# Performance work log

Hardware: AMD Instinct MI355X
Metric: run time of the kernel (lower is better)

Reference implementation:

```python
import jax, jax.numpy as jnp
import numpy as np

B, T, N, E = 4, 16, 1024, 16384
F_IN, H, FF, NH, L, C = 128, 256, 1024, 8, 2, 10
HD = H // NH
EPS = 1e-5


def setup_inputs() -> dict:
    key = jax.random.key(0)
    ks = jax.random.split(key, 12)
    g = lambda k, s: jax.random.normal(k, s, dtype=jnp.float32) * 0.02
    return {
        "x": jax.random.normal(ks[0], (B, T, N, F_IN), dtype=jnp.float32),
        "edge_index": jax.random.randint(ks[1], (B, T, 2, E), 0, N, dtype=jnp.int32),
        # GraphSAGE layer 1 (PyG SAGEConv: lin_l on mean-aggregated neighbors, lin_r on self)
        "sage1_Wl": g(ks[2], (F_IN, H)), "sage1_bl": jnp.zeros((H,), jnp.float32),
        "sage1_Wr": g(ks[3], (F_IN, H)),
        # GraphSAGE layer 2
        "sage2_Wl": g(ks[4], (H, H)), "sage2_bl": jnp.zeros((H,), jnp.float32),
        "sage2_Wr": g(ks[5], (H, H)),
        # TransformerEncoder, stacked over L layers
        "Wqkv": g(ks[6], (L, H, 3 * H)), "bqkv": jnp.zeros((L, 3 * H), jnp.float32),
        "Wo": g(ks[7], (L, H, H)), "bo": jnp.zeros((L, H), jnp.float32),
        "ln1_s": jnp.ones((L, H), jnp.float32), "ln1_b": jnp.zeros((L, H), jnp.float32),
        "W1": g(ks[8], (L, H, FF)), "b1": jnp.zeros((L, FF), jnp.float32),
        "W2": g(ks[9], (L, FF, H)), "b2": jnp.zeros((L, H), jnp.float32),
        "ln2_s": jnp.ones((L, H), jnp.float32), "ln2_b": jnp.zeros((L, H), jnp.float32),
        # final classifier
        "fc_W": g(ks[10], (H, C)), "fc_b": jnp.zeros((C,), jnp.float32),
    }


def _sage_conv(x, src, dst, Wl, bl, Wr):
    # mean neighbor aggregation: for each target node, mean of source features
    deg = jax.ops.segment_sum(jnp.ones((E,), x.dtype), dst, num_segments=N)
    agg = jax.ops.segment_sum(x[src], dst, num_segments=N)  # [N, F]
    agg = agg / jnp.clip(deg, 1.0)[:, None]
    return agg @ Wl + bl + x @ Wr


def _layernorm(x, s, b):
    m = jnp.mean(x, axis=-1, keepdims=True)
    v = jnp.var(x, axis=-1, keepdims=True)
    return (x - m) * jax.lax.rsqrt(v + EPS) * s + b


def _encoder_layer(h, Wqkv, bqkv, Wo, bo, ln1_s, ln1_b, W1, b1, W2, b2, ln2_s, ln2_b):
    # h: [B, T, H] -- post-norm (PyTorch default norm_first=False), relu FFN
    qkv = h @ Wqkv + bqkv  # [B, T, 3H]
    q, k, v = jnp.split(qkv, 3, axis=-1)
    sp = lambda t: t.reshape(B, T, NH, HD).transpose(0, 2, 1, 3)  # [B, NH, T, HD]
    q, k, v = sp(q), sp(k), sp(v)
    scores = jnp.einsum("bhqd,bhkd->bhqk", q, k) / np.sqrt(HD).astype(np.float32)
    attn = jax.nn.softmax(scores, axis=-1)
    ctx = jnp.einsum("bhqk,bhkd->bhqd", attn, v)
    ctx = ctx.transpose(0, 2, 1, 3).reshape(B, T, H)
    h = _layernorm(h + ctx @ Wo + bo, ln1_s, ln1_b)
    ffn = jax.nn.relu(h @ W1 + b1) @ W2 + b2
    return _layernorm(h + ffn, ln2_s, ln2_b)


def reference(x, edge_index, sage1_Wl, sage1_bl, sage1_Wr, sage2_Wl, sage2_bl,
              sage2_Wr, Wqkv, bqkv, Wo, bo, ln1_s, ln1_b, W1, b1, W2, b2,
              ln2_s, ln2_b, fc_W, fc_b):
    xf = x.reshape(B * T, N, F_IN)
    ef = edge_index.reshape(B * T, 2, E)

    def per_graph(xg, eg):
        src, dst = eg[0], eg[1]
        h = jax.nn.relu(_sage_conv(xg, src, dst, sage1_Wl, sage1_bl, sage1_Wr))
        h = _sage_conv(h, src, dst, sage2_Wl, sage2_bl, sage2_Wr)
        return jnp.mean(h, axis=0)  # mean-pool over nodes -> [H]

    emb = jax.vmap(per_graph)(xf, ef).reshape(B, T, H)

    h = emb
    for l in range(L):
        h = _encoder_layer(h, Wqkv[l], bqkv[l], Wo[l], bo[l], ln1_s[l], ln1_b[l],
                           W1[l], b1[l], W2[l], b2[l], ln2_s[l], ln2_b[l])
    return h[:, -1, :] @ fc_W + fc_b  # [B, C]
```

## Files before the change

kernel.cpp:

```cpp
#include <hip/hip_runtime.h>
#include <hip/hip_bf16.h>

#define Bc 4
#define Tc 16
#define Nc 1024
#define Ec 16384
#define FIN 128
#define Hc 256
#define FFc 1024
#define NHc 8
#define Lc 2
#define HDc 32
#define Gc 64
#define EPSc 1e-5f

typedef __bf16 v8bf __attribute__((ext_vector_type(8)));
typedef float v4f __attribute__((ext_vector_type(4)));

#define TREE256(red, tid, OUTVAR) {                                             \
    if ((tid) < 128) red[tid] += red[(tid) + 128];                              \
    __syncthreads();                                                            \
    if ((tid) < 64) {                                                           \
        float v_ = red[tid] + red[(tid) + 64];                                  \
        v_ += __shfl_down(v_, 32);                                              \
        v_ += __shfl_down(v_, 16);                                              \
        v_ += __shfl_down(v_, 8);                                               \
        v_ += __shfl_down(v_, 4);                                               \
        v_ += __shfl_down(v_, 2);                                               \
        v_ += __shfl_down(v_, 1);                                               \
        if ((tid) == 0) red[0] = v_;                                            \
    }                                                                           \
    __syncthreads();                                                            \
    OUTVAR = red[0];                                                            \
}

__global__ void pack_w_kernel(const float* __restrict__ Wl, const float* __restrict__ Wr,
                              __bf16* __restrict__ pH, __bf16* __restrict__ pL) {
    int bid = blockIdx.x;
    int t = threadIdx.x;
    int lane = t >> 3, j = t & 7;
    int kc = bid >> 4, nt = bid & 15;
    int k = kc * 32 + ((lane >> 4) << 3) + j;
    int n = nt * 16 + (lane & 15);
    float w = (k < 128) ? Wl[(size_t)k * Hc + n] : Wr[(size_t)(k - 128) * Hc + n];
    __bf16 hi = (__bf16)w;
    __bf16 lo = (__bf16)(w - (float)hi);
    pH[bid * 512 + t] = hi;
    pL[bid * 512 + t] = lo;
}

__global__ __launch_bounds__(1024) void csr_kernel(
        const int* __restrict__ ei, float* __restrict__ invdeg, float* __restrict__ cw,
        int* __restrict__ off, unsigned short* __restrict__ elist, float* __restrict__ uv) {
    __shared__ int degs[Nc];
    __shared__ float inv[Nc];
    __shared__ float cl[Nc];
    __shared__ int wsum[16];
    int g = blockIdx.x, t = threadIdx.x;
    const int* src = ei + (size_t)g * 2 * Ec;
    const int* dst = src + Ec;
    int ld[16], ls[16];
#pragma unroll
    for (int i = 0; i < 16; ++i) ld[i] = dst[t + i * 1024] & (Nc - 1);
#pragma unroll
    for (int i = 0; i < 16; ++i) ls[i] = src[t + i * 1024] & (Nc - 1);
    if (t < 512) uv[g * 512 + t] = 0.f;
    degs[t] = 0; cl[t] = 0.f;
    __syncthreads();
#pragma unroll
    for (int i = 0; i < 16; ++i) atomicAdd(&degs[ld[i]], 1);
    __syncthreads();
    float iv = 1.0f / fmaxf((float)degs[t], 1.0f);
    inv[t] = iv;
    invdeg[g * Nc + t] = iv;
    __syncthreads();
#pragma unroll
    for (int i = 0; i < 16; ++i) atomicAdd(&cl[ls[i]], inv[ld[i]]);
    __syncthreads();
    cw[g * Nc + t] = cl[t];
    int own = degs[t];
    int lane = t & 63, wv = t >> 6;
    int val = own;
#pragma unroll
    for (int ofs = 1; ofs < 64; ofs <<= 1) {
        int v = __shfl_up(val, ofs, 64);
        if (lane >= ofs) val += v;
    }
    if (lane == 63) wsum[wv] = val;
    __syncthreads();
    if (wv == 0 && lane < 16) {
        int wval = wsum[lane];
#pragma unroll
        for (int ofs = 1; ofs < 16; ofs <<= 1) {
            int v = __shfl_up(wval, ofs, 64);
            if (lane >= ofs) wval += v;
        }
        wsum[lane] = wval;
    }
    __syncthreads();
    int incl = val + ((wv > 0) ? wsum[wv - 1] : 0);
    int excl = incl - own;
    off[g * 1032 + t] = excl;
    if (t == 1023) off[g * 1032 + Nc] = incl;
    degs[t] = excl;
    __syncthreads();
#pragma unroll
    for (int i = 0; i < 16; ++i) {
        int slot = atomicAdd(&degs[ld[i]], 1);
        elist[(size_t)g * Ec + slot] = (unsigned short)ls[i];
    }
}

__global__ __launch_bounds__(512) void sage_kernel(
        const float* __restrict__ x, const unsigned short* __restrict__ elist,
        const int* __restrict__ off, const float* __restrict__ invdeg,
        const float* __restrict__ cw, const __bf16* __restrict__ pH,
        const __bf16* __restrict__ pL, const float* __restrict__ bias,
        float* __restrict__ uv) {
    __shared__ float aggL[32 * 132];
    __shared__ float xL[32 * 132];
    __shared__ float lu[256], lv[256];
    int tid = threadIdx.x;
    int bid = blockIdx.x;
    int g = bid & 63, cc = bid >> 6, r0 = cc * 32;
    const unsigned short* el = elist + (size_t)g * Ec;
    const float* xg = x + (size_t)g * Nc * FIN;
    if (tid < 256) { lu[tid] = 0.f; lv[tid] = 0.f; }

    {
        int lr = tid >> 4, ch = tid & 15;
        int n = r0 + lr;
        int o0 = off[g * 1032 + n], o1 = off[g * 1032 + n + 1];
        float4 a0 = make_float4(0.f, 0.f, 0.f, 0.f);
        float4 a1 = make_float4(0.f, 0.f, 0.f, 0.f);
        const float* xc = xg + ch * 8;
        int e = o0;
        for (; e + 8 <= o1; e += 8) {
            int s[8];
#pragma unroll
            for (int j = 0; j < 8; ++j) s[j] = el[e + j];
            float4 v0[8], v1[8];
#pragma unroll
            for (int j = 0; j < 8; ++j) {
                const float4* xp = (const float4*)(xc + (size_t)s[j] * FIN);
                v0[j] = xp[0]; v1[j] = xp[1];
            }
#pragma unroll
            for (int j = 0; j < 8; ++j) {
                a0.x += v0[j].x; a0.y += v0[j].y; a0.z += v0[j].z; a0.w += v0[j].w;
                a1.x += v1[j].x; a1.y += v1[j].y; a1.z += v1[j].z; a1.w += v1[j].w;
            }
        }
        for (; e < o1; ++e) {
            const float4* xp = (const float4*)(xc + (size_t)el[e] * FIN);
            float4 v0 = xp[0], v1 = xp[1];
            a0.x += v0.x; a0.y += v0.y; a0.z += v0.z; a0.w += v0.w;
            a1.x += v1.x; a1.y += v1.y; a1.z += v1.z; a1.w += v1.w;
        }
        float iv = invdeg[g * Nc + n];
        float* dp = &aggL[lr * 132 + ch * 8];
        dp[0] = a0.x * iv; dp[1] = a0.y * iv; dp[2] = a0.z * iv; dp[3] = a0.w * iv;
        dp[4] = a1.x * iv; dp[5] = a1.y * iv; dp[6] = a1.z * iv; dp[7] = a1.w * iv;
    }
    for (int i = tid; i < 1024; i += 512) {
        int lr = i >> 5, kq = i & 31;
        *(float4*)&xL[lr * 132 + kq * 4] = *(const float4*)&xg[(size_t)(r0 + lr) * FIN + kq * 4];
    }
    __syncthreads();

    int w = tid >> 6, lane = tid & 63, quad = lane >> 4;
    int mt = w & 1, nh = w >> 1;
    int lrow = mt * 16 + (lane & 15);
    v4f acc[4];
#pragma unroll
    for (int i = 0; i < 4; ++i) acc[i] = (v4f)0.f;
    for (int kc = 0; kc < 8; ++kc) {
        const float* ap = (kc < 4) ? &aggL[lrow * 132 + kc * 32 + quad * 8]
                                   : &xL[lrow * 132 + (kc - 4) * 32 + quad * 8];
        float4 f0 = *(const float4*)ap;
        float4 f1 = *(const float4*)(ap + 4);
        float av[8] = {f0.x, f0.y, f0.z, f0.w, f1.x, f1.y, f1.z, f1.w};
        v8bf aH, aL;
#pragma unroll
        for (int j = 0; j < 8; ++j) {
            __bf16 hb = (__bf16)av[j];
            aH[j] = hb;
            aL[j] = (__bf16)(av[j] - (float)hb);
        }
#pragma unroll
        for (int i = 0; i < 4; ++i) {
            int nt = nh * 4 + i;
            v8bf bH = *(const v8bf*)(pH + ((size_t)(kc * 16 + nt) * 64 + lane) * 8);
            v8bf bL = *(const v8bf*)(pL + ((size_t)(kc * 16 + nt) * 64 + lane) * 8);
            acc[i] = __builtin_amdgcn_mfma_f32_16x16x32_bf16(aH, bH, acc[i], 0, 0, 0);
            acc[i] = __builtin_amdgcn_mfma_f32_16x16x32_bf16(aL, bH, acc[i], 0, 0, 0);
            acc[i] = __builtin_amdgcn_mfma_f32_16x16x32_bf16(aH, bL, acc[i], 0, 0, 0);
        }
    }

    float c4[4];
    int nb = g * Nc + r0 + mt * 16 + quad * 4;
#pragma unroll
    for (int r = 0; r < 4; ++r) c4[r] = cw[nb + r];
#pragma unroll
    for (int i = 0; i < 4; ++i) {
        int col = (nh * 4 + i) * 16 + (lane & 15);
        float bcol = bias[col];
        float su = 0.f, sv = 0.f;
#pragma unroll
        for (int r = 0; r < 4; ++r) {
            float val = fmaxf(acc[i][r] + bcol, 0.f);
            sv += val;
            su += c4[r] * val;
        }
        su += __shfl_xor(su, 16); sv += __shfl_xor(sv, 16);
        su += __shfl_xor(su, 32); sv += __shfl_xor(sv, 32);
        if (quad == 0) { atomicAdd(&lu[col], su); atomicAdd(&lv[col], sv); }
    }
    __syncthreads();
    if (tid < 256) {
        atomicAdd(&uv[g * 512 + tid], lu[tid]);
        atomicAdd(&uv[g * 512 + 256 + tid], lv[tid]);
    }
}

__global__ __launch_bounds__(512) void emb_kernel(
        const float* __restrict__ uv, const float* __restrict__ Wl2,
        const float* __restrict__ bl2, const float* __restrict__ Wr2,
        float* __restrict__ h) {
    __shared__ float s[512];
    __shared__ float r2[512];
    int g = blockIdx.x, tid = threadIdx.x;
    s[tid] = uv[g * 512 + tid] * (1.0f / Nc);
    __syncthreads();
    int col = tid & 255, p = tid >> 8;
    float val = 0.f;
    if (p == 0) { for (int k = 0; k < 256; ++k) val += s[k] * Wl2[(size_t)k * Hc + col]; }
    else        { for (int k = 0; k < 256; ++k) val += s[256 + k] * Wr2[(size_t)k * Hc + col]; }
    r2[tid] = val;
    __syncthreads();
    if (tid < 256) h[g * Hc + tid] = bl2[tid] + r2[tid] + r2[tid + 256];
}

__global__ __launch_bounds__(512) void qkv_kernel(
        const float* __restrict__ h, const float* __restrict__ Wqkv,
        const float* __restrict__ bqkv, float* __restrict__ qkv, int l) {
    __shared__ float hr[256];
    __shared__ float r2[512];
    int bid = blockIdx.x;
    int gi = bid / 3, seg = bid % 3;
    int tid = threadIdx.x;
    if (tid < 256) hr[tid] = h[gi * Hc + tid];
    __syncthreads();
    int col = seg * 256 + (tid & 255);
    int half = tid >> 8;
    const float* W = Wqkv + (size_t)l * Hc * 768;
    float val = 0.f;
    int k0 = half * 128;
    for (int k = 0; k < 128; ++k) val += hr[k0 + k] * W[(size_t)(k0 + k) * 768 + col];
    r2[tid] = val;
    __syncthreads();
    if (tid < 256) qkv[gi * 768 + col] = bqkv[(size_t)l * 768 + col] + r2[tid] + r2[tid + 256];
}

#define KVS 516
__global__ __launch_bounds__(1024) void rest_kernel(
        const float* __restrict__ hin, float* __restrict__ hout,
        const float* __restrict__ qkvg,
        const float* __restrict__ Wo, const float* __restrict__ bo,
        const float* __restrict__ s1, const float* __restrict__ b1ln,
        const float* __restrict__ W1, const float* __restrict__ bf1,
        const float* __restrict__ W2, const float* __restrict__ bf2,
        const float* __restrict__ s2, const float* __restrict__ b2ln,
        const float* __restrict__ fcW, const float* __restrict__ fcb,
        float* __restrict__ out, int l, int last) {
    __shared__ float kv[16 * KVS];
    __shared__ float q[256];
    __shared__ float sc[8][17];
    __shared__ float ctx[256];
    __shared__ float r2[512];
    __shared__ float red[256];
    __shared__ float rF[2048];
    __shared__ float fLs[1024];
    __shared__ float h1L[256];
    int t = blockIdx.x, tid = threadIdx.x;
    int b = t >> 4;
    const float* qb = qkvg + (size_t)(b * 16) * 768;
    for (int i = tid; i < 8192; i += 1024) {
        int j = i >> 9, d = i & 511;
        kv[j * KVS + d] = qb[(size_t)j * 768 + 256 + d];
    }
    if (tid < 256) q[tid] = qkvg[(size_t)t * 768 + tid];
    __syncthreads();
    if (tid < 128) {
        int hd = tid >> 4, jj = tid & 15;
        float s = 0.f;
#pragma unroll
        for (int d = 0; d < 32; ++d) s += q[hd * 32 + d] * kv[jj * KVS + hd * 32 + d];
        sc[hd][jj] = s * 0.17677669529663687f;
    }
    __syncthreads();
    if (tid < 8) {
        float m = sc[tid][0];
        for (int j = 1; j < 16; ++j) m = fmaxf(m, sc[tid][j]);
        float e[16], sum = 0.f;
        for (int j = 0; j < 16; ++j) { e[j] = expf(sc[tid][j] - m); sum += e[j]; }
        float inv = 1.0f / sum;
        for (int j = 0; j < 16; ++j) sc[tid][j] = e[j] * inv;
    }
    __syncthreads();
    if (tid < 256) {
        int hd = tid >> 5, d = tid & 31;
        float o = 0.f;
#pragma unroll
        for (int j = 0; j < 16; ++j) o += sc[hd][j] * kv[j * KVS + 256 + hd * 32 + d];
        ctx[tid] = o;
    }
    __syncthreads();
    if (tid < 512) {
        int col = tid & 255, half = tid >> 8;
        const float* W = Wo + (size_t)l * 65536;
        float pv = 0.f;
        int k0 = half * 128;
        for (int k = 0; k < 128; ++k) pv += ctx[k0 + k] * W[(size_t)(k0 + k) * 256 + col];
        r2[tid] = pv;
    }
    __syncthreads();
    float val = 0.f;
    if (tid < 256) {
        val = hin[(size_t)t * 256 + tid] + bo[(size_t)l * 256 + tid] + r2[tid] + r2[tid + 256];
        red[tid] = val;
    }
    __syncthreads();
    float sm1; TREE256(red, tid, sm1);
    float m1 = sm1 * (1.0f / 256.0f);
    __syncthreads();
    float d1 = val - m1;
    if (tid < 256) red[tid] = d1 * d1;
    __syncthreads();
    float sv1; TREE256(red, tid, sv1);
    float v1 = sv1 * (1.0f / 256.0f);
    if (tid < 256)
        h1L[tid] = d1 * rsqrtf(v1 + EPSc) * s1[(size_t)l * 256 + tid] + b1ln[(size_t)l * 256 + tid];
    __syncthreads();
#pragma unroll
    for (int pass = 0; pass < 2; ++pass) {
        int pid = pass * 1024 + tid;
        int cg = pid >> 9, ch = pid & 511;
        int col = cg * 256 + (ch & 255), half = ch >> 8;
        const float* W = W1 + (size_t)l * 262144;
        float v = 0.f;
        int k0 = half * 128;
        for (int k = 0; k < 128; ++k) v += h1L[k0 + k] * W[(size_t)(k0 + k) * 1024 + col];
        rF[pid] = v;
    }
    __syncthreads();
    {
        int cg = tid >> 8, c8 = tid & 255;
        fLs[tid] = fmaxf(bf1[(size_t)l * 1024 + tid] + rF[cg * 512 + c8] + rF[cg * 512 + 256 + c8], 0.f);
    }
    __syncthreads();
    {
        int col = tid & 255, kq = tid >> 8;
        const float* W = W2 + (size_t)l * 262144;
        float p = 0.f;
        int k0 = kq * 256;
        for (int k = 0; k < 256; ++k) p += fLs[k0 + k] * W[(size_t)(k0 + k) * 256 + col];
        rF[tid] = p;
    }
    __syncthreads();
    float val2 = 0.f;
    if (tid < 256) {
        val2 = h1L[tid] + bf2[(size_t)l * 256 + tid]
             + rF[tid] + rF[tid + 256] + rF[tid + 512] + rF[tid + 768];
        red[tid] = val2;
    }
    __syncthreads();
    float sm2; TREE256(red, tid, sm2);
    float m2 = sm2 * (1.0f / 256.0f);
    __syncthreads();
    float d2 = (tid < 256) ? (val2 - m2) : 0.f;
    if (tid < 256) red[tid] = d2 * d2;
    __syncthreads();
    float sv2; TREE256(red, tid, sv2);
    float var2 = sv2 * (1.0f / 256.0f);
    float hn = 0.f;
    if (tid < 256) {
        hn = d2 * rsqrtf(var2 + EPSc) * s2[(size_t)l * 256 + tid] + b2ln[(size_t)l * 256 + tid];
        hout[(size_t)t * 256 + tid] = hn;
    }
    if (last && (t & 15) == 15) {
        __syncthreads();
        if (tid < 256) red[tid] = hn;
        __syncthreads();
        if (tid < 10) {
            int bb = t >> 4;
            float fv = fcb[tid];
            for (int k = 0; k < 256; ++k) fv += red[k] * fcW[(size_t)k * 10 + tid];
            out[bb * 10 + tid] = fv;
        }
    }
}

extern "C" void kernel_launch(void* const* d_in, const int* in_sizes, int n_in,
                              void* d_out, int out_size, void* d_ws, size_t ws_size,
                              hipStream_t stream) {
    (void)in_sizes; (void)n_in; (void)out_size; (void)ws_size;
    const float* x    = (const float*)d_in[0];
    const int*   ei   = (const int*)d_in[1];
    const float* s1Wl = (const float*)d_in[2];
    const float* s1bl = (const float*)d_in[3];
    const float* s1Wr = (const float*)d_in[4];
    const float* s2Wl = (const float*)d_in[5];
    const float* s2bl = (const float*)d_in[6];
    const float* s2Wr = (const float*)d_in[7];
    const float* Wqkv = (const float*)d_in[8];
    const float* bqkv = (const float*)d_in[9];
    const float* Wo   = (const float*)d_in[10];
    const float* bo   = (const float*)d_in[11];
    const float* ln1s = (const float*)d_in[12];
    const float* ln1b = (const float*)d_in[13];
    const float* W1   = (const float*)d_in[14];
    const float* b1   = (const float*)d_in[15];
    const float* W2   = (const float*)d_in[16];
    const float* b2   = (const float*)d_in[17];
    const float* ln2s = (const float*)d_in[18];
    const float* ln2b = (const float*)d_in[19];
    const float* fcW  = (const float*)d_in[20];
    const float* fcb  = (const float*)d_in[21];

    char* ws = (char*)d_ws;
    __bf16*         packWH = (__bf16*)(ws + 0);
    __bf16*         packWL = (__bf16*)(ws + 131072);
    float*          invdeg = (float*)(ws + 262144);
    float*          cw     = (float*)(ws + 524288);
    int*            off    = (int*)(ws + 786432);
    unsigned short* elist  = (unsigned short*)(ws + 1050624);
    float*          uv     = (float*)(ws + 3147776);
    float*          h      = (float*)(ws + 3278848);
    float*          h2     = (float*)(ws + 3344384);
    float*          qkvg   = (float*)(ws + 3409920);

    pack_w_kernel<<<128, 512, 0, stream>>>(s1Wl, s1Wr, packWH, packWL);
    csr_kernel<<<Gc, 1024, 0, stream>>>(ei, invdeg, cw, off, elist, uv);
    sage_kernel<<<Gc * 32, 512, 0, stream>>>(x, elist, off, invdeg, cw, packWH, packWL, s1bl, uv);
    emb_kernel<<<Gc, 512, 0, stream>>>(uv, s2Wl, s2bl, s2Wr, h);
    qkv_kernel<<<Gc * 3, 512, 0, stream>>>(h, Wqkv, bqkv, qkvg, 0);
    rest_kernel<<<Gc, 1024, 0, stream>>>(h, h2, qkvg, Wo, bo, ln1s, ln1b,
                                         W1, b1, W2, b2, ln2s, ln2b, fcW, fcb,
                                         (float*)d_out, 0, 0);
    qkv_kernel<<<Gc * 3, 512, 0, stream>>>(h2, Wqkv, bqkv, qkvg, 1);
    rest_kernel<<<Gc, 1024, 0, stream>>>(h2, h, qkvg, Wo, bo, ln1s, ln1b,
                                         W1, b1, W2, b2, ln2s, ln2b, fcW, fcb,
                                         (float*)d_out, 1, 1);
}
```

Before: 312.9 us.

## Split transformer rest kernel into attention, FFN1, FFN2, and LN2 kernels

Breaks the per-token fused rest kernel into four kernels. Attention plus LN1 writes h1 in both row and transposed layouts. The FFN matmuls are then parallelised across output columns, with each block computing 8 columns for all 64 tokens, so every weight element is read once instead of once per token block. This targets redundant weight traffic in the 64-block per-token design, at the cost of extra launches and global round-trips for intermediates. The workspace regions reused for intermediates overlap the packed SAGE weights, which are already consumed by this point.

```diff
diff --git a/kernel.cpp b/kernel.cpp
--- a/kernel.cpp
+++ b/kernel.cpp
@@ -264,29 +264,21 @@
 }
 
 #define KVS 516
-__global__ __launch_bounds__(1024) void rest_kernel(
-        const float* __restrict__ hin, float* __restrict__ hout,
-        const float* __restrict__ qkvg,
+__global__ __launch_bounds__(512) void apl_kernel(
+        const float* __restrict__ h, const float* __restrict__ qkvg,
         const float* __restrict__ Wo, const float* __restrict__ bo,
         const float* __restrict__ s1, const float* __restrict__ b1ln,
-        const float* __restrict__ W1, const float* __restrict__ bf1,
-        const float* __restrict__ W2, const float* __restrict__ bf2,
-        const float* __restrict__ s2, const float* __restrict__ b2ln,
-        const float* __restrict__ fcW, const float* __restrict__ fcb,
-        float* __restrict__ out, int l, int last) {
+        float* __restrict__ h1buf, float* __restrict__ h1bufT, int l) {
     __shared__ float kv[16 * KVS];
     __shared__ float q[256];
     __shared__ float sc[8][17];
     __shared__ float ctx[256];
     __shared__ float r2[512];
     __shared__ float red[256];
-    __shared__ float rF[2048];
-    __shared__ float fLs[1024];
-    __shared__ float h1L[256];
     int t = blockIdx.x, tid = threadIdx.x;
     int b = t >> 4;
     const float* qb = qkvg + (size_t)(b * 16) * 768;
-    for (int i = tid; i < 8192; i += 1024) {
+    for (int i = tid; i < 8192; i += 512) {
         int j = i >> 9, d = i & 511;
         kv[j * KVS + d] = qb[(size_t)j * 768 + 256 + d];
     }
@@ -317,7 +309,7 @@
         ctx[tid] = o;
     }
     __syncthreads();
-    if (tid < 512) {
+    {
         int col = tid & 255, half = tid >> 8;
         const float* W = Wo + (size_t)l * 65536;
         float pv = 0.f;
@@ -328,7 +320,7 @@
     __syncthreads();
     float val = 0.f;
     if (tid < 256) {
-        val = hin[(size_t)t * 256 + tid] + bo[(size_t)l * 256 + tid] + r2[tid] + r2[tid + 256];
+        val = h[(size_t)t * 256 + tid] + bo[(size_t)l * 256 + tid] + r2[tid] + r2[tid + 256];
         red[tid] = val;
     }
     __syncthreads();
@@ -340,58 +332,70 @@
     __syncthreads();
     float sv1; TREE256(red, tid, sv1);
     float v1 = sv1 * (1.0f / 256.0f);
-    if (tid < 256)
-        h1L[tid] = d1 * rsqrtf(v1 + EPSc) * s1[(size_t)l * 256 + tid] + b1ln[(size_t)l * 256 + tid];
-    __syncthreads();
-#pragma unroll
-    for (int pass = 0; pass < 2; ++pass) {
-        int pid = pass * 1024 + tid;
-        int cg = pid >> 9, ch = pid & 511;
-        int col = cg * 256 + (ch & 255), half = ch >> 8;
-        const float* W = W1 + (size_t)l * 262144;
-        float v = 0.f;
-        int k0 = half * 128;
-        for (int k = 0; k < 128; ++k) v += h1L[k0 + k] * W[(size_t)(k0 + k) * 1024 + col];
-        rF[pid] = v;
-    }
-    __syncthreads();
-    {
-        int cg = tid >> 8, c8 = tid & 255;
-        fLs[tid] = fmaxf(bf1[(size_t)l * 1024 + tid] + rF[cg * 512 + c8] + rF[cg * 512 + 256 + c8], 0.f);
-    }
-    __syncthreads();
-    {
-        int col = tid & 255, kq = tid >> 8;
-        const float* W = W2 + (size_t)l * 262144;
-        float p = 0.f;
+    if (tid < 256) {
+        float hv = d1 * rsqrtf(v1 + EPSc) * s1[(size_t)l * 256 + tid] + b1ln[(size_t)l * 256 + tid];
+        h1buf[(size_t)t * 256 + tid] = hv;
+        h1bufT[(size_t)tid * 64 + t] = hv;
+    }
+}
+
+__global__ __launch_bounds__(512) void ffn1_kernel(
+        const float* __restrict__ h1bufT, const float* __restrict__ W1,
+        const float* __restrict__ bf1, float* __restrict__ fLT, int l) {
+    int bid = blockIdx.x, tid = threadIdx.x;
+    int cl = tid >> 6, t = tid & 63;
+    int col = bid * 8 + cl;
+    const float* W = W1 + (size_t)l * 262144 + col;
+    float p0 = 0.f, p1 = 0.f;
+    for (int k = 0; k < 128; ++k)  p0 += h1bufT[k * 64 + t] * W[(size_t)k * 1024];
+    for (int k = 128; k < 256; ++k) p1 += h1bufT[k * 64 + t] * W[(size_t)k * 1024];
+    fLT[(size_t)col * 64 + t] = fmaxf(bf1[(size_t)l * 1024 + col] + p0 + p1, 0.f);
+}
+
+__global__ __launch_bounds__(512) void ffn2_kernel(
+        const float* __restrict__ fLT, const float* __restrict__ W2,
+        const float* __restrict__ h1buf, const float* __restrict__ bf2,
+        float* __restrict__ val2g, int l) {
+    int bid = blockIdx.x, tid = threadIdx.x;
+    int cl = tid >> 6, t = tid & 63;
+    int col = bid * 8 + cl;
+    const float* W = W2 + (size_t)l * 262144 + col;
+    float p[4];
+#pragma unroll
+    for (int kq = 0; kq < 4; ++kq) {
+        float s = 0.f;
         int k0 = kq * 256;
-        for (int k = 0; k < 256; ++k) p += fLs[k0 + k] * W[(size_t)(k0 + k) * 256 + col];
-        rF[tid] = p;
-    }
-    __syncthreads();
-    float val2 = 0.f;
-    if (tid < 256) {
-        val2 = h1L[tid] + bf2[(size_t)l * 256 + tid]
-             + rF[tid] + rF[tid + 256] + rF[tid + 512] + rF[tid + 768];
-        red[tid] = val2;
-    }
+        for (int k = 0; k < 256; ++k)
+            s += fLT[(size_t)(k0 + k) * 64 + t] * W[(size_t)(k0 + k) * 256];
+        p[kq] = s;
+    }
+    val2g[(size_t)t * 256 + col] = h1buf[(size_t)t * 256 + col] + bf2[(size_t)l * 256 + col]
+                                 + p[0] + p[1] + p[2] + p[3];
+}
+
+__global__ __launch_bounds__(256) void ln2_kernel(
+        const float* __restrict__ val2g, float* __restrict__ hout,
+        const float* __restrict__ s2, const float* __restrict__ b2ln,
+        const float* __restrict__ fcW, const float* __restrict__ fcb,
+        float* __restrict__ out, int l, int last) {
+    __shared__ float red[256];
+    int t = blockIdx.x, tid = threadIdx.x;
+    float val2 = val2g[(size_t)t * 256 + tid];
+    red[tid] = val2;
     __syncthreads();
     float sm2; TREE256(red, tid, sm2);
     float m2 = sm2 * (1.0f / 256.0f);
     __syncthreads();
-    float d2 = (tid < 256) ? (val2 - m2) : 0.f;
-    if (tid < 256) red[tid] = d2 * d2;
+    float d2 = val2 - m2;
+    red[tid] = d2 * d2;
     __syncthreads();
     float sv2; TREE256(red, tid, sv2);
     float var2 = sv2 * (1.0f / 256.0f);
-    float hn = 0.f;
-    if (tid < 256) {
-        hn = d2 * rsqrtf(var2 + EPSc) * s2[(size_t)l * 256 + tid] + b2ln[(size_t)l * 256 + tid];
-        hout[(size_t)t * 256 + tid] = hn;
-    }
+    float hn = d2 * rsqrtf(var2 + EPSc) * s2[(size_t)l * 256 + tid] + b2ln[(size_t)l * 256 + tid];
+    hout[(size_t)t * 256 + tid] = hn;
     if (last && (t & 15) == 15) {
         __syncthreads();
-        if (tid < 256) red[tid] = hn;
+        red[tid] = hn;
         __syncthreads();
         if (tid < 10) {
             int bb = t >> 4;
@@ -440,17 +444,23 @@
     float*          h      = (float*)(ws + 3278848);
     float*          h2     = (float*)(ws + 3344384);
     float*          qkvg   = (float*)(ws + 3409920);
+    float*          h1buf  = (float*)(ws + 0);
+    float*          h1bufT = (float*)(ws + 65536);
+    float*          fLT    = (float*)(ws + 131072);
+    float*          val2g  = (float*)(ws + 393216);
 
     pack_w_kernel<<<128, 512, 0, stream>>>(s1Wl, s1Wr, packWH, packWL);
     csr_kernel<<<Gc, 1024, 0, stream>>>(ei, invdeg, cw, off, elist, uv);
     sage_kernel<<<Gc * 32, 512, 0, stream>>>(x, elist, off, invdeg, cw, packWH, packWL, s1bl, uv);
     emb_kernel<<<Gc, 512, 0, stream>>>(uv, s2Wl, s2bl, s2Wr, h);
-    qkv_kernel<<<Gc * 3, 512, 0, stream>>>(h, Wqkv, bqkv, qkvg, 0);
-    rest_kernel<<<Gc, 1024, 0, stream>>>(h, h2, qkvg, Wo, bo, ln1s, ln1b,
-                                         W1, b1, W2, b2, ln2s, ln2b, fcW, fcb,
-                                         (float*)d_out, 0, 0);
-    qkv_kernel<<<Gc * 3, 512, 0, stream>>>(h2, Wqkv, bqkv, qkvg, 1);
-    rest_kernel<<<Gc, 1024, 0, stream>>>(h2, h, qkvg, Wo, bo, ln1s, ln1b,
-                                         W1, b1, W2, b2, ln2s, ln2b, fcW, fcb,
-                                         (float*)d_out, 1, 1);
-}
+    for (int l = 0; l < Lc; ++l) {
+        const float* hin = (l == 0) ? h : h2;
+        float* hout = (l == 0) ? h2 : h;
+        qkv_kernel<<<Gc * 3, 512, 0, stream>>>(hin, Wqkv, bqkv, qkvg, l);
+        apl_kernel<<<Gc, 512, 0, stream>>>(hin, qkvg, Wo, bo, ln1s, ln1b, h1buf, h1bufT, l);
+        ffn1_kernel<<<128, 512, 0, stream>>>(h1bufT, W1, b1, fLT, l);
+        ffn2_kernel<<<32, 512, 0, stream>>>(fLT, W2, h1buf, b2, val2g, l);
+        ln2_kernel<<<Gc, 256, 0, stream>>>(val2g, hout, ln2s, ln2b, fcW, fcb,
+                                           (float*)d_out, l, l == Lc - 1);
+    }
+}
```

Measured after the change: 402.5 us. 28.6% more time.
